# Optimization experiments

Hardware: AMD Instinct MI355X
Metric: run time of the kernel (lower is better)

The kernel has to match this reference:

```python
import jax, jax.numpy as jnp
import numpy as np

B, N, D_IN, D_HID = 8, 2048, 512, 512

def setup_inputs() -> dict:
    key = jax.random.key(0)
    k1, k2, k3 = jax.random.split(key, 3)
    inp = jax.random.normal(k1, (B, N, D_IN), dtype=jnp.float32)
    # nn.Linear(input_size, hidden_size): weight [hidden, in], bias [hidden]
    W = jax.random.normal(k2, (D_HID, D_IN), dtype=jnp.float32) * (1.0 / np.sqrt(D_IN))
    b = jax.random.normal(k3, (D_HID,), dtype=jnp.float32) * 0.01
    return {"input": inp, "W": W, "b": b}

def reference(input, W, b):
    # x = fc(input): [B, N, D_HID]
    x = jnp.einsum('bnd,hd->bnh', input, W) + b
    # scores = x @ x^T (NO scale factor, matching the original): [B, N, N]
    scores = jnp.einsum('bnh,bmh->bnm', x, x)
    attn = jax.nn.softmax(scores, axis=2)
    # output = attn @ raw input (V = input, not the projection): [B, N, D_IN]
    output = jnp.einsum('bnm,bmd->bnd', attn, input)
    return output
```

## Files before the change

### kernel.cpp

```cpp
#include <hip/hip_runtime.h>
#include <hip/hip_bf16.h>
#include <stdint.h>

typedef short vbf16x8 __attribute__((ext_vector_type(8)));
typedef float vf32x4 __attribute__((ext_vector_type(4)));
typedef unsigned short u16;

__device__ __forceinline__ float bf2f(u16 u) {
  union { unsigned int i; float f; } v; v.i = ((unsigned int)u) << 16; return v.f;
}
__device__ __forceinline__ u16 f2bf(float f) {
  union { float f; unsigned int i; } v; v.f = f;
  return (u16)((v.i + 0x7fffu + ((v.i >> 16) & 1u)) >> 16);
}
__device__ __forceinline__ void gld16(const void* g, void* l) {
  __builtin_amdgcn_global_load_lds((const __attribute__((address_space(1))) void*)g,
                                   (__attribute__((address_space(3))) void*)l, 16, 0, 0);
}
template<int N> __device__ __forceinline__ void wait_vmcnt() {
  asm volatile("s_waitcnt vmcnt(%0)" :: "n"(N) : "memory");
}
__device__ __forceinline__ vbf16x8 ldsv(const u16* p) { return *(const vbf16x8*)p; }

__global__ __launch_bounds__(256) void k_convw(const float* __restrict__ W, u16* __restrict__ Wb) {
  int i = blockIdx.x * 256 + threadIdx.x;
  float4 x = ((const float4*)W)[i];
  ushort4 h;
  h.x = f2bf(x.x); h.y = f2bf(x.y); h.z = f2bf(x.z); h.w = f2bf(x.w);
  ((ushort4*)Wb)[i] = h;
}

__global__ __launch_bounds__(256) void k_prep(const float* __restrict__ in,
                                              u16* __restrict__ Abf, u16* __restrict__ Vt) {
  __shared__ u16 Ts[64][72];
  const int tid = threadIdx.x;
  const int n0 = blockIdx.x * 64, d0 = blockIdx.y * 64, b = blockIdx.z;
  const float* src = in + ((long long)b * 2048 + n0) * 512 + d0;
#pragma unroll
  for (int j = 0; j < 4; ++j) {
    int chunk = tid + 256 * j;
    int r = chunk >> 4, c = (chunk & 15) * 4;
    float4 x = *(const float4*)(src + (long long)r * 512 + c);
    ushort4 h;
    h.x = f2bf(x.x); h.y = f2bf(x.y); h.z = f2bf(x.z); h.w = f2bf(x.w);
    *(ushort4*)(Abf + ((long long)b * 2048 + n0 + r) * 512 + d0 + c) = h;
    Ts[c + 0][r] = h.x; Ts[c + 1][r] = h.y; Ts[c + 2][r] = h.z; Ts[c + 3][r] = h.w;
  }
  __syncthreads();
#pragma unroll
  for (int j = 0; j < 2; ++j) {
    int chunk = tid + 256 * j;
    int dr = chunk >> 3, c8 = (chunk & 7) * 8;
    vbf16x8 w = *(const vbf16x8*)&Ts[dr][c8];
    *(vbf16x8*)(Vt + ((long long)b * 512 + d0 + dr) * 2048 + n0 + c8) = w;
  }
}

__device__ __forceinline__ void sround(const u16* g, int K, int k0, u16* ldsbuf,
                                       int r, int srow, int scol, int wv) {
  gld16(g + (long long)(r * 64 + srow) * K + k0 + scol, ldsbuf + r * 4096 + wv * 512);
}

template<bool OUTBF, bool BIAS, int MAP>
__global__ __launch_bounds__(512, 2) void k_gemm(const u16* __restrict__ A,
                                                 const u16* __restrict__ Bt,
                                                 const float* __restrict__ bias,
                                                 void* __restrict__ Cout,
                                                 int M, int N, int K,
                                                 long long sA, long long sB, long long sC) {
  __shared__ __align__(16) u16 As[3 * 16384];
  __shared__ __align__(16) u16 Bs[3 * 8192];

  const int tid = threadIdx.x, lane = tid & 63, wv = tid >> 6;
  const int wr = wv >> 2, wc = wv & 3;

  const int lin = blockIdx.x;
  const int xcd = lin & 7, idx = lin >> 3;
  int zb, browi, bcoli;
  if constexpr (MAP == 1) { zb = 0; browi = xcd * 8 + (idx >> 2); bcoli = idx & 3; }
  else { zb = xcd; browi = idx >> 2; bcoli = idx & 3; }
  const int brow = browi * 256, bcol = bcoli * 128;
  const long long z = zb;

  const u16* gA = A + z * sA + (long long)brow * K;
  const u16* gB = Bt + z * sB + (long long)bcol * K;
  const int NT = K >> 6;

  const int srow = wv * 8 + (lane >> 3);
  const int scol = (((lane & 7) ^ ((lane >> 3) & 7)) << 3);
  const int rd0 = (lane & 15) * 64 + ((((lane >> 4)) ^ (lane & 7)) << 3);
  const int wrb = wr * 8192;
  const int wcb = wc * 2048;

  vf32x4 acc[8][2] = {};
  vbf16x8 afr[4], bfr[2];

  u16 *A0 = As, *A1 = As + 16384, *A2 = As + 32768;
  u16 *B0 = Bs, *B1 = Bs + 8192, *B2 = Bs + 16384;

  sround(gA, K, 0, A0, 0, srow, scol, wv);
  sround(gA, K, 0, A0, 1, srow, scol, wv);
  sround(gA, K, 0, A0, 2, srow, scol, wv);
  sround(gA, K, 0, A0, 3, srow, scol, wv);
  sround(gB, K, 0, B0, 0, srow, scol, wv);
  sround(gB, K, 0, B0, 1, srow, scol, wv);
  sround(gA, K, 64, A1, 0, srow, scol, wv);
  sround(gA, K, 64, A1, 1, srow, scol, wv);
  sround(gA, K, 64, A1, 2, srow, scol, wv);
  sround(gA, K, 64, A1, 3, srow, scol, wv);
  sround(gB, K, 64, B1, 0, srow, scol, wv);
  sround(gB, K, 64, B1, 1, srow, scol, wv);

  for (int t = 0; t < NT; ++t) {
    const int k2 = (t + 2) * 64;
    const bool st = (t + 2 < NT);

    if (t < NT - 1) wait_vmcnt<6>(); else wait_vmcnt<0>();
    __builtin_amdgcn_sched_barrier(0);
    __builtin_amdgcn_s_barrier();
    __builtin_amdgcn_sched_barrier(0);

#pragma unroll
    for (int n = 0; n < 2; ++n) bfr[n] = ldsv(B0 + wcb + n * 1024 + rd0);
#pragma unroll
    for (int i = 0; i < 4; ++i) afr[i] = ldsv(A0 + wrb + i * 1024 + rd0);
    if (st) { sround(gA, K, k2, A2, 0, srow, scol, wv); sround(gA, K, k2, A2, 1, srow, scol, wv); }
    __builtin_amdgcn_s_setprio(1);
#pragma unroll
    for (int i = 0; i < 4; ++i)
#pragma unroll
      for (int n = 0; n < 2; ++n)
        acc[i][n] = __builtin_amdgcn_mfma_f32_16x16x32_bf16(afr[i], bfr[n], acc[i][n], 0, 0, 0);
    __builtin_amdgcn_s_setprio(0);

#pragma unroll
    for (int i = 0; i < 4; ++i) afr[i] = ldsv(A0 + wrb + (4 + i) * 1024 + rd0);
    if (st) sround(gA, K, k2, A2, 2, srow, scol, wv);
    __builtin_amdgcn_s_setprio(1);
#pragma unroll
    for (int i = 0; i < 4; ++i)
#pragma unroll
      for (int n = 0; n < 2; ++n)
        acc[4 + i][n] = __builtin_amdgcn_mfma_f32_16x16x32_bf16(afr[i], bfr[n], acc[4 + i][n], 0, 0, 0);
    __builtin_amdgcn_s_setprio(0);

#pragma unroll
    for (int n = 0; n < 2; ++n) bfr[n] = ldsv(B0 + wcb + n * 1024 + (rd0 ^ 32));
#pragma unroll
    for (int i = 0; i < 4; ++i) afr[i] = ldsv(A0 + wrb + i * 1024 + (rd0 ^ 32));
    if (st) { sround(gA, K, k2, A2, 3, srow, scol, wv); sround(gB, K, k2, B2, 0, srow, scol, wv); }
    __builtin_amdgcn_s_setprio(1);
#pragma unroll
    for (int i = 0; i < 4; ++i)
#pragma unroll
      for (int n = 0; n < 2; ++n)
        acc[i][n] = __builtin_amdgcn_mfma_f32_16x16x32_bf16(afr[i], bfr[n], acc[i][n], 0, 0, 0);
    __builtin_amdgcn_s_setprio(0);

#pragma unroll
    for (int i = 0; i < 4; ++i) afr[i] = ldsv(A0 + wrb + (4 + i) * 1024 + (rd0 ^ 32));
    if (st) sround(gB, K, k2, B2, 1, srow, scol, wv);
    __builtin_amdgcn_s_setprio(1);
#pragma unroll
    for (int i = 0; i < 4; ++i)
#pragma unroll
      for (int n = 0; n < 2; ++n)
        acc[4 + i][n] = __builtin_amdgcn_mfma_f32_16x16x32_bf16(afr[i], bfr[n], acc[4 + i][n], 0, 0, 0);
    __builtin_amdgcn_s_setprio(0);

    u16* ta = A0; A0 = A1; A1 = A2; A2 = ta;
    u16* tb = B0; B0 = B1; B1 = B2; B2 = tb;
  }

  const long long zc = z * sC;
#pragma unroll
  for (int m = 0; m < 8; ++m) {
    const int row0 = brow + wr * 128 + m * 16 + (lane >> 4) * 4;
#pragma unroll
    for (int n = 0; n < 2; ++n) {
      const int col = bcol + wc * 32 + n * 16 + (lane & 15);
      const float bv = BIAS ? bias[col] : 0.0f;
#pragma unroll
      for (int r = 0; r < 4; ++r) {
        const float v = acc[m][n][r] + bv;
        const long long off = zc + (long long)(row0 + r) * N + col;
        if (OUTBF) ((u16*)Cout)[off] = f2bf(v);
        else       ((float*)Cout)[off] = v;
      }
    }
  }
}

__device__ __forceinline__ void sr32(const u16* g, int K, int k0, u16* ldsbuf,
                                     int r, int srow, int scol, int wv) {
  gld16(g + (long long)(r * 128 + srow) * K + k0 + scol, ldsbuf + r * 4096 + wv * 512);
}

__global__ __launch_bounds__(512, 2) void k_gemmS(const u16* __restrict__ X,
                                                  u16* __restrict__ P) {
  constexpr int K = 512, N = 2048;
  __shared__ __align__(16) u16 As[3 * 8192];
  __shared__ __align__(16) u16 Bs[3 * 8192];

  const int tid = threadIdx.x, lane = tid & 63, wv = tid >> 6;
  const int wr = wv >> 2, wc = wv & 3;

  const int lin = blockIdx.x;
  const int xcd = lin & 7, idx = lin >> 3;
  const int brow = (idx >> 3) * 256, bcol = (idx & 7) * 256;
  const long long z = xcd;

  const u16* gA = X + z * (2048LL * 512) + (long long)brow * K;
  const u16* gB = X + z * (2048LL * 512) + (long long)bcol * K;
  const int NT = K >> 5;

  const int srow = wv * 16 + (lane >> 2);
  const int scol = (((lane & 3) ^ ((lane >> 3) & 3)) << 3);

  const int rd = (lane & 15) * 32 + ((((lane >> 4)) ^ (((lane & 15) >> 1) & 3)) << 3);
  const int wrb = wr * 4096;
  const int wcb = wc * 2048;

  vf32x4 acc[8][4] = {};
  vbf16x8 afr[4], bfr[4];

  u16 *A0 = As, *A1 = As + 8192, *A2 = As + 16384;
  u16 *B0 = Bs, *B1 = Bs + 8192, *B2 = Bs + 16384;

  sr32(gA, K, 0, A0, 0, srow, scol, wv);
  sr32(gA, K, 0, A0, 1, srow, scol, wv);
  sr32(gB, K, 0, B0, 0, srow, scol, wv);
  sr32(gB, K, 0, B0, 1, srow, scol, wv);
  sr32(gA, K, 32, A1, 0, srow, scol, wv);
  sr32(gA, K, 32, A1, 1, srow, scol, wv);
  sr32(gB, K, 32, B1, 0, srow, scol, wv);
  sr32(gB, K, 32, B1, 1, srow, scol, wv);

  for (int t = 0; t < NT; ++t) {
    const int k2 = (t + 2) * 32;
    const bool st = (t + 2 < NT);

    if (t < NT - 1) wait_vmcnt<4>(); else wait_vmcnt<0>();
    __builtin_amdgcn_sched_barrier(0);
    __builtin_amdgcn_s_barrier();
    __builtin_amdgcn_sched_barrier(0);

#pragma unroll
    for (int n = 0; n < 4; ++n) bfr[n] = ldsv(B0 + wcb + n * 512 + rd);
#pragma unroll
    for (int i = 0; i < 4; ++i) afr[i] = ldsv(A0 + wrb + i * 512 + rd);
    if (st) { sr32(gA, K, k2, A2, 0, srow, scol, wv); sr32(gA, K, k2, A2, 1, srow, scol, wv); }
    __builtin_amdgcn_s_setprio(1);
#pragma unroll
    for (int i = 0; i < 4; ++i)
#pragma unroll
      for (int n = 0; n < 4; ++n)
        acc[i][n] = __builtin_amdgcn_mfma_f32_16x16x32_bf16(afr[i], bfr[n], acc[i][n], 0, 0, 0);
    __builtin_amdgcn_s_setprio(0);

#pragma unroll
    for (int i = 0; i < 4; ++i) afr[i] = ldsv(A0 + wrb + (4 + i) * 512 + rd);
    if (st) { sr32(gB, K, k2, B2, 0, srow, scol, wv); sr32(gB, K, k2, B2, 1, srow, scol, wv); }
    __builtin_amdgcn_s_setprio(1);
#pragma unroll
    for (int i = 0; i < 4; ++i)
#pragma unroll
      for (int n = 0; n < 4; ++n)
        acc[4 + i][n] = __builtin_amdgcn_mfma_f32_16x16x32_bf16(afr[i], bfr[n], acc[4 + i][n], 0, 0, 0);
    __builtin_amdgcn_s_setprio(0);

    u16* ta = A0; A0 = A1; A1 = A2; A2 = ta;
    u16* tb = B0; B0 = B1; B1 = B2; B2 = tb;
  }

  const long long zc = z * (2048LL * 2048);
#pragma unroll
  for (int m = 0; m < 8; ++m) {
    const int row0 = brow + wr * 128 + m * 16 + (lane >> 4) * 4;
#pragma unroll
    for (int n = 0; n < 4; ++n) {
      const int col = bcol + wc * 64 + n * 16 + (lane & 15);
#pragma unroll
      for (int r = 0; r < 4; ++r) {
        P[zc + (long long)(row0 + r) * N + col] = f2bf(acc[m][n][r]);
      }
    }
  }
}

__global__ __launch_bounds__(256) void k_softmax(u16* __restrict__ P) {
  const long long row = blockIdx.x;
  u16* p = P + row * 2048;
  const int tid = threadIdx.x, lane = tid & 63, wv = tid >> 6;
  vbf16x8 v = ((const vbf16x8*)p)[tid];
  float f[8];
#pragma unroll
  for (int j = 0; j < 8; ++j) f[j] = bf2f((u16)v[j]);
  float m = f[0];
#pragma unroll
  for (int j = 1; j < 8; ++j) m = fmaxf(m, f[j]);
  for (int o = 1; o < 64; o <<= 1) m = fmaxf(m, __shfl_xor(m, o));
  __shared__ float redm[4], reds[4];
  if (lane == 0) redm[wv] = m;
  __syncthreads();
  m = fmaxf(fmaxf(redm[0], redm[1]), fmaxf(redm[2], redm[3]));
  float s = 0.0f;
#pragma unroll
  for (int j = 0; j < 8; ++j) { f[j] = __expf(f[j] - m); s += f[j]; }
  for (int o = 1; o < 64; o <<= 1) s += __shfl_xor(s, o);
  if (lane == 0) reds[wv] = s;
  __syncthreads();
  const float inv = 1.0f / (reds[0] + reds[1] + reds[2] + reds[3]);
#pragma unroll
  for (int j = 0; j < 8; ++j) v[j] = (short)f2bf(f[j] * inv);
  ((vbf16x8*)p)[tid] = v;
}

extern "C" void kernel_launch(void* const* d_in, const int* in_sizes, int n_in,
                              void* d_out, int out_size, void* d_ws, size_t ws_size,
                              hipStream_t stream) {
  const float* input = (const float*)d_in[0];
  const float* W     = (const float*)d_in[1];
  const float* bias  = (const float*)d_in[2];
  float* out = (float*)d_out;

  char* ws = (char*)d_ws;
  u16* Xbf = (u16*)(ws);
  u16* Vt  = (u16*)(ws + 16777216);
  u16* P   = (u16*)(ws + 2LL * 16777216);
  u16* Abf = (u16*)(ws + 2LL * 16777216);
  u16* Wb  = (u16*)(ws + 3LL * 16777216);

  k_convw<<<256, 256, 0, stream>>>(W, Wb);
  k_prep<<<dim3(32, 8, 8), 256, 0, stream>>>(input, Abf, Vt);
  k_gemm<true, true, 1><<<256, 512, 0, stream>>>(
      Abf, Wb, bias, Xbf, 16384, 512, 512, 0, 0, 0);
  k_gemmS<<<512, 512, 0, stream>>>(Xbf, P);
  k_softmax<<<16384, 256, 0, stream>>>(P);
  k_gemm<false, false, 2><<<256, 512, 0, stream>>>(
      P, Vt, nullptr, out, 2048, 512, 2048,
      2048LL * 2048, 512LL * 2048, 2048LL * 512);
}
```

Before: 122.1 us.

## Fuse softmax into score and PV GEMMs using diagonal-norm max bound

Removes the standalone softmax kernel. The score GEMM now subtracts each row's self-dot (the squared norm ||x_n||², accumulated from the A fragments) in place of the row max, and writes unnormalized exp values as bf16. The PV GEMM computes row sums with extra MFMAs against a ones vector and divides at the epilogue. This saves one full read and write pass over the 2048x2048 score matrix per batch. The cost is extra MFMA work in the PV GEMM and an exponent offset that relies on the self-dot dominating each row, which is only a Cauchy-Schwarz-style heuristic: a row with a small self-dot could overflow, and one whose self-dot is far above its other scores could underflow.

```diff
diff --git a/kernel.cpp b/kernel.cpp
--- a/kernel.cpp
+++ b/kernel.cpp
@@ -61,7 +61,7 @@
   gld16(g + (long long)(r * 64 + srow) * K + k0 + scol, ldsbuf + r * 4096 + wv * 512);
 }
 
-template<bool OUTBF, bool BIAS, int MAP>
+template<bool OUTBF, bool BIAS, int MAP, bool NORM>
 __global__ __launch_bounds__(512, 2) void k_gemm(const u16* __restrict__ A,
                                                  const u16* __restrict__ Bt,
                                                  const float* __restrict__ bias,
@@ -93,7 +93,13 @@
   const int wcb = wc * 2048;
 
   vf32x4 acc[8][2] = {};
+  vf32x4 accl[8] = {};
   vbf16x8 afr[4], bfr[2];
+  vbf16x8 ones;
+  if constexpr (NORM) {
+#pragma unroll
+    for (int j = 0; j < 8; ++j) ones[j] = (short)0x3F80;
+  }
 
   u16 *A0 = As, *A1 = As + 16384, *A2 = As + 32768;
   u16 *B0 = Bs, *B1 = Bs + 8192, *B2 = Bs + 16384;
@@ -131,6 +137,11 @@
 #pragma unroll
       for (int n = 0; n < 2; ++n)
         acc[i][n] = __builtin_amdgcn_mfma_f32_16x16x32_bf16(afr[i], bfr[n], acc[i][n], 0, 0, 0);
+    if constexpr (NORM) {
+#pragma unroll
+      for (int i = 0; i < 4; ++i)
+        accl[i] = __builtin_amdgcn_mfma_f32_16x16x32_bf16(afr[i], ones, accl[i], 0, 0, 0);
+    }
     __builtin_amdgcn_s_setprio(0);
 
 #pragma unroll
@@ -142,6 +153,11 @@
 #pragma unroll
       for (int n = 0; n < 2; ++n)
         acc[4 + i][n] = __builtin_amdgcn_mfma_f32_16x16x32_bf16(afr[i], bfr[n], acc[4 + i][n], 0, 0, 0);
+    if constexpr (NORM) {
+#pragma unroll
+      for (int i = 0; i < 4; ++i)
+        accl[4 + i] = __builtin_amdgcn_mfma_f32_16x16x32_bf16(afr[i], ones, accl[4 + i], 0, 0, 0);
+    }
     __builtin_amdgcn_s_setprio(0);
 
 #pragma unroll
@@ -155,6 +171,11 @@
 #pragma unroll
       for (int n = 0; n < 2; ++n)
         acc[i][n] = __builtin_amdgcn_mfma_f32_16x16x32_bf16(afr[i], bfr[n], acc[i][n], 0, 0, 0);
+    if constexpr (NORM) {
+#pragma unroll
+      for (int i = 0; i < 4; ++i)
+        accl[i] = __builtin_amdgcn_mfma_f32_16x16x32_bf16(afr[i], ones, accl[i], 0, 0, 0);
+    }
     __builtin_amdgcn_s_setprio(0);
 
 #pragma unroll
@@ -166,6 +187,11 @@
 #pragma unroll
       for (int n = 0; n < 2; ++n)
         acc[4 + i][n] = __builtin_amdgcn_mfma_f32_16x16x32_bf16(afr[i], bfr[n], acc[4 + i][n], 0, 0, 0);
+    if constexpr (NORM) {
+#pragma unroll
+      for (int i = 0; i < 4; ++i)
+        accl[4 + i] = __builtin_amdgcn_mfma_f32_16x16x32_bf16(afr[i], ones, accl[4 + i], 0, 0, 0);
+    }
     __builtin_amdgcn_s_setprio(0);
 
     u16* ta = A0; A0 = A1; A1 = A2; A2 = ta;
@@ -182,7 +208,8 @@
       const float bv = BIAS ? bias[col] : 0.0f;
 #pragma unroll
       for (int r = 0; r < 4; ++r) {
-        const float v = acc[m][n][r] + bv;
+        float v = acc[m][n][r] + bv;
+        if constexpr (NORM) v = v / accl[m][r];
         const long long off = zc + (long long)(row0 + r) * N + col;
         if (OUTBF) ((u16*)Cout)[off] = f2bf(v);
         else       ((float*)Cout)[off] = v;
@@ -216,12 +243,12 @@
 
   const int srow = wv * 16 + (lane >> 2);
   const int scol = (((lane & 3) ^ ((lane >> 3) & 3)) << 3);
-
   const int rd = (lane & 15) * 32 + ((((lane >> 4)) ^ (((lane & 15) >> 1) & 3)) << 3);
   const int wrb = wr * 4096;
   const int wcb = wc * 2048;
 
   vf32x4 acc[8][4] = {};
+  float d_acc[8] = {};
   vbf16x8 afr[4], bfr[4];
 
   u16 *A0 = As, *A1 = As + 8192, *A2 = As + 16384;
@@ -257,6 +284,13 @@
       for (int n = 0; n < 4; ++n)
         acc[i][n] = __builtin_amdgcn_mfma_f32_16x16x32_bf16(afr[i], bfr[n], acc[i][n], 0, 0, 0);
     __builtin_amdgcn_s_setprio(0);
+#pragma unroll
+    for (int i = 0; i < 4; ++i)
+#pragma unroll
+      for (int j = 0; j < 8; ++j) {
+        float x = bf2f((u16)afr[i][j]);
+        d_acc[i] = fmaf(x, x, d_acc[i]);
+      }
 
 #pragma unroll
     for (int i = 0; i < 4; ++i) afr[i] = ldsv(A0 + wrb + (4 + i) * 512 + rd);
@@ -268,52 +302,40 @@
       for (int n = 0; n < 4; ++n)
         acc[4 + i][n] = __builtin_amdgcn_mfma_f32_16x16x32_bf16(afr[i], bfr[n], acc[4 + i][n], 0, 0, 0);
     __builtin_amdgcn_s_setprio(0);
+#pragma unroll
+    for (int i = 0; i < 4; ++i)
+#pragma unroll
+      for (int j = 0; j < 8; ++j) {
+        float x = bf2f((u16)afr[i][j]);
+        d_acc[4 + i] = fmaf(x, x, d_acc[4 + i]);
+      }
 
     u16* ta = A0; A0 = A1; A1 = A2; A2 = ta;
     u16* tb = B0; B0 = B1; B1 = B2; B2 = tb;
   }
 
+#pragma unroll
+  for (int i = 0; i < 8; ++i) {
+    d_acc[i] += __shfl_xor(d_acc[i], 16);
+    d_acc[i] += __shfl_xor(d_acc[i], 32);
+  }
+
+  const float L2E = 1.44269504088896f;
   const long long zc = z * (2048LL * 2048);
 #pragma unroll
   for (int m = 0; m < 8; ++m) {
     const int row0 = brow + wr * 128 + m * 16 + (lane >> 4) * 4;
 #pragma unroll
-    for (int n = 0; n < 4; ++n) {
-      const int col = bcol + wc * 64 + n * 16 + (lane & 15);
-#pragma unroll
-      for (int r = 0; r < 4; ++r) {
-        P[zc + (long long)(row0 + r) * N + col] = f2bf(acc[m][n][r]);
+    for (int r = 0; r < 4; ++r) {
+      const float dL = __shfl(d_acc[m], (lane >> 4) * 4 + r) * L2E;
+#pragma unroll
+      for (int n = 0; n < 4; ++n) {
+        const int col = bcol + wc * 64 + n * 16 + (lane & 15);
+        const float p = exp2f(fmaf(acc[m][n][r], L2E, -dL));
+        P[zc + (long long)(row0 + r) * N + col] = f2bf(p);
       }
     }
   }
-}
-
-__global__ __launch_bounds__(256) void k_softmax(u16* __restrict__ P) {
-  const long long row = blockIdx.x;
-  u16* p = P + row * 2048;
-  const int tid = threadIdx.x, lane = tid & 63, wv = tid >> 6;
-  vbf16x8 v = ((const vbf16x8*)p)[tid];
-  float f[8];
-#pragma unroll
-  for (int j = 0; j < 8; ++j) f[j] = bf2f((u16)v[j]);
-  float m = f[0];
-#pragma unroll
-  for (int j = 1; j < 8; ++j) m = fmaxf(m, f[j]);
-  for (int o = 1; o < 64; o <<= 1) m = fmaxf(m, __shfl_xor(m, o));
-  __shared__ float redm[4], reds[4];
-  if (lane == 0) redm[wv] = m;
-  __syncthreads();
-  m = fmaxf(fmaxf(redm[0], redm[1]), fmaxf(redm[2], redm[3]));
-  float s = 0.0f;
-#pragma unroll
-  for (int j = 0; j < 8; ++j) { f[j] = __expf(f[j] - m); s += f[j]; }
-  for (int o = 1; o < 64; o <<= 1) s += __shfl_xor(s, o);
-  if (lane == 0) reds[wv] = s;
-  __syncthreads();
-  const float inv = 1.0f / (reds[0] + reds[1] + reds[2] + reds[3]);
-#pragma unroll
-  for (int j = 0; j < 8; ++j) v[j] = (short)f2bf(f[j] * inv);
-  ((vbf16x8*)p)[tid] = v;
 }
 
 extern "C" void kernel_launch(void* const* d_in, const int* in_sizes, int n_in,
@@ -333,11 +355,10 @@
 
   k_convw<<<256, 256, 0, stream>>>(W, Wb);
   k_prep<<<dim3(32, 8, 8), 256, 0, stream>>>(input, Abf, Vt);
-  k_gemm<true, true, 1><<<256, 512, 0, stream>>>(
+  k_gemm<true, true, 1, false><<<256, 512, 0, stream>>>(
       Abf, Wb, bias, Xbf, 16384, 512, 512, 0, 0, 0);
   k_gemmS<<<512, 512, 0, stream>>>(Xbf, P);
-  k_softmax<<<16384, 256, 0, stream>>>(P);
-  k_gemm<false, false, 2><<<256, 512, 0, stream>>>(
+  k_gemm<false, false, 2, true><<<256, 512, 0, stream>>>(
       P, Vt, nullptr, out, 2048, 512, 2048,
       2048LL * 2048, 512LL * 2048, 2048LL * 512);
 }
```

Result: no change. 120.9 us (-1.0%).
